# Performance work log

Measured on AMD Instinct MI355X. Metric: run time of the kernel, lower is better.

The kernel has to match this reference:

```python
import jax, jax.numpy as jnp
import numpy as np

DEPTH, HEADS, DIM_HEAD, DIM = 6, 16, 64, 1024
INNER = HEADS * DIM_HEAD  # 1024 == DIM
MLP = DIM                 # mlp_dim chosen == dim (see shape_source)
SCALE = DIM_HEAD ** -0.5
EPS = 1e-5


def _layernorm(x, w, b):
    m = jnp.mean(x, axis=-1, keepdims=True)
    v = jnp.mean(jnp.square(x - m), axis=-1, keepdims=True)
    return (x - m) * jax.lax.rsqrt(v + EPS) * w + b


def _rpq_weight(cb, codes):
    # cb: [G, 256, sub], codes: [out, G] -> W: [out, G*sub] == [out, in]
    G = cb.shape[0]
    W = cb[jnp.arange(G)[None, :], codes]  # [out, G, sub]
    return W.reshape(codes.shape[0], -1)


def _rpq_linear(x, cb, codes, b=None):
    W = _rpq_weight(cb, codes)
    y = jnp.einsum('bni,oi->bno', x, W)
    return y if b is None else y + b


def setup_inputs() -> dict:
    key = jax.random.key(0)
    ks = jax.random.split(key, 17)
    cs = 0.02  # codebook scale (kaiming-uniform-ish magnitude)
    return {
        'x': jax.random.normal(ks[0], (8, 1024, DIM), jnp.float32),
        'cb0': jax.random.normal(ks[1], (HEADS, 256, DIM // HEADS), jnp.float32) * cs,
        'cb1': jax.random.normal(ks[2], (HEADS, 256, DIM // HEADS), jnp.float32) * cs,
        'cb2': jax.random.normal(ks[3], (HEADS, 256, MLP // HEADS), jnp.float32) * cs,
        'cb3': jax.random.normal(ks[4], (HEADS, 256, MLP // HEADS), jnp.float32) * cs,
        'codes_qkv': jax.random.randint(ks[5], (DEPTH, 3 * INNER, HEADS), 0, 256, jnp.int32),
        'codes_out': jax.random.randint(ks[6], (DEPTH, DIM, HEADS), 0, 256, jnp.int32),
        'codes_fc1': jax.random.randint(ks[7], (DEPTH, MLP, HEADS), 0, 256, jnp.int32),
        'codes_fc2': jax.random.randint(ks[8], (DEPTH, DIM, HEADS), 0, 256, jnp.int32),
        'b_out': jax.random.normal(ks[9], (DEPTH, DIM), jnp.float32) * 0.02,
        'b_fc1': jax.random.normal(ks[10], (DEPTH, MLP), jnp.float32) * 0.02,
        'b_fc2': jax.random.normal(ks[11], (DEPTH, DIM), jnp.float32) * 0.02,
        'ln1_w': jax.random.uniform(ks[12], (DEPTH, DIM), jnp.float32, 0.5, 1.5),
        'ln1_b': jax.random.normal(ks[13], (DEPTH, DIM), jnp.float32) * 0.02,
        'ln2_w': jax.random.uniform(ks[14], (DEPTH, DIM), jnp.float32, 0.5, 1.5),
        'ln2_b': jax.random.normal(ks[15], (DEPTH, DIM), jnp.float32) * 0.02,
    }


def reference(x, cb0, cb1, cb2, cb3, codes_qkv, codes_out, codes_fc1, codes_fc2,
              b_out, b_fc1, b_fc2, ln1_w, ln1_b, ln2_w, ln2_b):
    b, n, _ = x.shape
    for i in range(DEPTH):
        # PreNorm Attention
        xn = _layernorm(x, ln1_w[i], ln1_b[i])
        qkv = _rpq_linear(xn, cb0, codes_qkv[i])  # [b, n, 3*INNER]
        q, k, v = jnp.split(qkv, 3, axis=-1)
        q = q.reshape(b, n, HEADS, DIM_HEAD).transpose(0, 2, 1, 3)  # bhnd
        k = k.reshape(b, n, HEADS, DIM_HEAD).transpose(0, 2, 1, 3)
        v = v.reshape(b, n, HEADS, DIM_HEAD).transpose(0, 2, 1, 3)
        dots = jnp.einsum('bhqd,bhkd->bhqk', q, k) * SCALE
        attn = jax.nn.softmax(dots, axis=-1)
        out = jnp.einsum('bhqk,bhkd->bhqd', attn, v)
        out = out.transpose(0, 2, 1, 3).reshape(b, n, INNER)
        out = _rpq_linear(out, cb1, codes_out[i], b_out[i])
        x = out + x
        # PreNorm FeedForward
        xn = _layernorm(x, ln2_w[i], ln2_b[i])
        h = jax.nn.gelu(_rpq_linear(xn, cb2, codes_fc1[i], b_fc1[i]), approximate=False)
        x = _rpq_linear(h, cb3, codes_fc2[i], b_fc2[i]) + x
    return x
```

## Files before the change

kernel.cpp:

```cpp
#include <hip/hip_runtime.h>
#include <hip/hip_bf16.h>


typedef __bf16 bf16x8 __attribute__((ext_vector_type(8)));
typedef __bf16 bf16x4 __attribute__((ext_vector_type(4)));
typedef float  f32x4  __attribute__((ext_vector_type(4)));
typedef float  f32x16 __attribute__((ext_vector_type(16)));
typedef unsigned int u32x4 __attribute__((ext_vector_type(4)));
typedef unsigned int u32_as1 __attribute__((address_space(1)));
typedef unsigned int u32_as3 __attribute__((address_space(3)));

#define MFMA16(a, b, c) __builtin_amdgcn_mfma_f32_16x16x32_bf16(a, b, c, 0, 0, 0)
#define MFMA32(a, b, c) __builtin_amdgcn_mfma_f32_32x32x16_bf16(a, b, c, 0, 0, 0)

__device__ __forceinline__ void gload16(void* lds, const void* g) {
  __builtin_amdgcn_global_load_lds((u32_as1*)(void*)g, (u32_as3*)lds, 16, 0, 0);
}

__device__ __forceinline__ unsigned pack2(float a, float b) {
  unsigned lo = (unsigned)__builtin_bit_cast(unsigned short, (__bf16)a);
  unsigned hi = (unsigned)__builtin_bit_cast(unsigned short, (__bf16)b);
  return lo | (hi << 16);
}
__device__ __forceinline__ void pswap(unsigned& a, unsigned& b) {
  asm("v_permlane32_swap_b32 %0, %1" : "+v"(a), "+v"(b));
}

__global__ __launch_bounds__(256) void dequant_kernel(
    __bf16* __restrict__ W,
    const float* __restrict__ cb0, const float* __restrict__ cb1,
    const float* __restrict__ cb2, const float* __restrict__ cb3,
    const int* __restrict__ codes_qkv, const int* __restrict__ codes_out,
    const int* __restrict__ codes_fc1, const int* __restrict__ codes_fc2)
{
  const int r = blockIdx.x;
  const int t = threadIdx.x;
  const float* cb; const int* cr;
  if (r < 3072)      { cb = cb0; cr = codes_qkv + r * 16; }
  else if (r < 4096) { cb = cb1; cr = codes_out + (r - 3072) * 16; }
  else if (r < 5120) { cb = cb2; cr = codes_fc1 + (r - 4096) * 16; }
  else               { cb = cb3; cr = codes_fc2 + (r - 5120) * 16; }
  const int g = t >> 4, j = (t & 15) * 4;
  const int code = cr[g];
  const float4 v = *(const float4*)(cb + ((size_t)(g * 256 + code) * 64) + j);
  bf16x4 o = { (__bf16)v.x, (__bf16)v.y, (__bf16)v.z, (__bf16)v.w };
  *(bf16x4*)(W + (size_t)r * 1024 + g * 64 + j) = o;
}

__global__ __launch_bounds__(256) void ln_kernel(
    const float* __restrict__ x, const float* __restrict__ w,
    const float* __restrict__ b, __bf16* __restrict__ out)
{
  const int row = blockIdx.x, t = threadIdx.x;
  const float4 v = *(const float4*)(x + (size_t)row * 1024 + t * 4);
  float s  = v.x + v.y + v.z + v.w;
  float sq = v.x * v.x + v.y * v.y + v.z * v.z + v.w * v.w;
  #pragma unroll
  for (int off = 32; off > 0; off >>= 1) {
    s  += __shfl_xor(s,  off, 64);
    sq += __shfl_xor(sq, off, 64);
  }
  __shared__ float red[8];
  const int wid = t >> 6, lane = t & 63;
  if (lane == 0) { red[wid] = s; red[4 + wid] = sq; }
  __syncthreads();
  s  = red[0] + red[1] + red[2] + red[3];
  sq = red[4] + red[5] + red[6] + red[7];
  const float mean = s * (1.0f / 1024.0f);
  const float var  = sq * (1.0f / 1024.0f) - mean * mean;
  const float rstd = rsqrtf(var + 1e-5f);
  const float4 wv = *(const float4*)(w + t * 4);
  const float4 bv = *(const float4*)(b + t * 4);
  bf16x4 o = { (__bf16)((v.x - mean) * rstd * wv.x + bv.x),
               (__bf16)((v.y - mean) * rstd * wv.y + bv.y),
               (__bf16)((v.z - mean) * rstd * wv.z + bv.z),
               (__bf16)((v.w - mean) * rstd * wv.w + bv.w) };
  *(bf16x4*)(out + (size_t)row * 1024 + t * 4) = o;
}

template<int EPI>
__global__ __launch_bounds__(256) void gemm_kernel(
    const __bf16* __restrict__ A, const __bf16* __restrict__ Bw,
    __bf16* __restrict__ oQ, __bf16* __restrict__ oK, __bf16* __restrict__ oVT,
    __bf16* __restrict__ oH, float* __restrict__ oX, const float* __restrict__ bias)
{
  __shared__ char smem[16384] __attribute__((aligned(128)));
  const int tid  = threadIdx.x;
  const int lane = tid & 63, wid = tid >> 6;
  const int l15 = lane & 15, l4 = lane >> 4;
  const int wr = wid >> 1, wc = wid & 1;
  const int m0 = blockIdx.x * 128, n0 = blockIdx.y * 128;

  const int srow = tid >> 2;
  const int scol = (tid & 3) * 8;

  f32x4 acc[4][4];
  #pragma unroll
  for (int i = 0; i < 4; ++i)
    #pragma unroll
    for (int j = 0; j < 4; ++j) acc[i][j] = (f32x4){0.f, 0.f, 0.f, 0.f};

  const __bf16* gA = A  + (size_t)(m0 + srow) * 1024 + scol;
  const __bf16* gB = Bw + (size_t)(n0 + srow) * 1024 + scol;
  char* ldsA0 = smem + wid * 1024;
  char* ldsA1 = smem + 4096  + wid * 1024;
  char* ldsB0 = smem + 8192  + wid * 1024;
  char* ldsB1 = smem + 12288 + wid * 1024;
  const int aoff = l15 * 64 + l4 * 16;

  for (int kk = 0; kk < 32; ++kk) {
    const int kb = kk * 32;
    gload16(ldsA0, gA + kb);
    gload16(ldsA1, gA + 64 * 1024 + kb);
    gload16(ldsB0, gB + kb);
    gload16(ldsB1, gB + 64 * 1024 + kb);
    __syncthreads();
    bf16x8 af[4], bfr[4];
    #pragma unroll
    for (int mi = 0; mi < 4; ++mi)
      af[mi] = *(const bf16x8*)(smem + (wr * 64 + mi * 16) * 64 + aoff);
    #pragma unroll
    for (int ni = 0; ni < 4; ++ni)
      bfr[ni] = *(const bf16x8*)(smem + 8192 + (wc * 64 + ni * 16) * 64 + aoff);
    #pragma unroll
    for (int mi = 0; mi < 4; ++mi)
      #pragma unroll
      for (int ni = 0; ni < 4; ++ni)
        acc[mi][ni] = MFMA16(af[mi], bfr[ni], acc[mi][ni]);
    __syncthreads();
  }

  #pragma unroll
  for (int mi = 0; mi < 4; ++mi) {
    #pragma unroll
    for (int ni = 0; ni < 4; ++ni) {
      const int n = n0 + wc * 64 + ni * 16 + l15;
      if constexpr (EPI == 0) {
        const int region = n >> 10, nn = n & 1023;
        const int hh = nn >> 6, d = nn & 63;
        const int m_base = m0 + wr * 64 + mi * 16 + l4 * 4;
        const int bb = m_base >> 10, s = m_base & 1023;
        if (region == 2) {
          bf16x4 pv = { (__bf16)acc[mi][ni][0], (__bf16)acc[mi][ni][1],
                        (__bf16)acc[mi][ni][2], (__bf16)acc[mi][ni][3] };
          *(bf16x4*)(oVT + ((size_t)(bb * 16 + hh) * 64 + d) * 1024 + s) = pv;
        } else {
          #pragma unroll
          for (int r = 0; r < 4; ++r) {
            const __bf16 bv = (__bf16)acc[mi][ni][r];
            if (region == 0) oQ[((size_t)(bb * 16 + hh) * 1024 + s + r) * 64 + d] = bv;
            else             oK[((size_t)(bb * 16 + hh) * 1024 + s + r) * 64 + d] = bv;
          }
        }
      } else {
        #pragma unroll
        for (int r = 0; r < 4; ++r) {
          const int m = m0 + wr * 64 + mi * 16 + l4 * 4 + r;
          const float v = acc[mi][ni][r];
          if constexpr (EPI == 1) {
            float* p = oX + (size_t)m * 1024 + n;
            *p = *p + v + bias[n];
          } else {
            float t = v + bias[n];
            t = 0.5f * t * (1.0f + erff(t * 0.70710678118f));
            oH[(size_t)m * 1024 + n] = (__bf16)t;
          }
        }
      }
    }
  }
}

__global__ __launch_bounds__(256) void attn_kernel(
    const __bf16* __restrict__ Q, const __bf16* __restrict__ K,
    const __bf16* __restrict__ VT, __bf16* __restrict__ AO)
{
  const int bh = blockIdx.x & 127;
  const int qt = blockIdx.x >> 7;
  const int tid = threadIdx.x, lane = tid & 63, wid = tid >> 6;
  const int l31 = lane & 31, hi = lane >> 5;
  const int q0 = qt * 128 + wid * 32;

  const __bf16* Qb = Q  + (size_t)bh * 65536;
  const __bf16* Kb = K  + (size_t)bh * 65536;
  const __bf16* Vb = VT + (size_t)bh * 65536;

  __shared__ char lds[2][16384] __attribute__((aligned(128)));

  const float ascale = 0.125f * 1.44269504089f;

  const int srow_in_chunk = lane >> 3;
  const int scol = (((lane & 7) ^ srow_in_chunk) << 3);

  #define STAGE(buf, kb_)                                                            \
    {                                                                                \
      _Pragma("unroll")                                                              \
      for (int ii = 0; ii < 4; ++ii) {                                               \
        const int i = wid + ii * 4;                                                  \
        const int chunk = i & 7;                                                     \
        const int row = chunk * 8 + srow_in_chunk;                                   \
        if (ii < 2) gload16((buf) + chunk * 1024,                                    \
                            Kb + (size_t)((kb_) + row) * 64 + scol);                 \
        else        gload16((buf) + 8192 + chunk * 1024,                             \
                            Vb + (size_t)row * 1024 + (kb_) + scol);                 \
      }                                                                              \
    }

  bf16x8 qf[4];
  #pragma unroll
  for (int c = 0; c < 4; ++c)
    qf[c] = *(const bf16x8*)(Qb + (size_t)(q0 + l31) * 64 + c * 16 + hi * 8);

  const u32x4 onesu = { 0x3f803f80u, 0x3f803f80u, 0x3f803f80u, 0x3f803f80u };
  const bf16x8 ones = __builtin_bit_cast(bf16x8, onesu);

  f32x16 o0, o1, sacc;
  #pragma unroll
  for (int r = 0; r < 16; ++r) { o0[r] = 0.f; o1[r] = 0.f; sacc[r] = 0.f; }
  float m = -1e30f;

  const int swz = (l31 & 7) << 4;

  STAGE(lds[0], 0);

  for (int kt = 0; kt < 16; ++kt) {
    __syncthreads();
    const char* Kl = lds[kt & 1];
    const char* Vl = lds[kt & 1] + 8192;
    if (kt < 15) STAGE(lds[(kt + 1) & 1], (kt + 1) * 64);

    f32x16 s0, s1;
    #pragma unroll
    for (int r = 0; r < 16; ++r) { s0[r] = 0.f; s1[r] = 0.f; }
    __builtin_amdgcn_s_setprio(1);
    #pragma unroll
    for (int c = 0; c < 4; ++c) {
      bf16x8 kf0 = *(const bf16x8*)(Kl + l31 * 128        + ((c * 32 + hi * 16) ^ swz));
      bf16x8 kf1 = *(const bf16x8*)(Kl + (32 + l31) * 128 + ((c * 32 + hi * 16) ^ swz));
      s0 = MFMA32(kf0, qf[c], s0);
      s1 = MFMA32(kf1, qf[c], s1);
    }
    __builtin_amdgcn_s_setprio(0);
    float t0 = fmaxf(s0[0], s0[1]),  t1 = fmaxf(s0[2], s0[3]);
    float t2 = fmaxf(s0[4], s0[5]),  t3 = fmaxf(s0[6], s0[7]);
    float t4 = fmaxf(s0[8], s0[9]),  t5 = fmaxf(s0[10], s0[11]);
    float t6 = fmaxf(s0[12], s0[13]), t7 = fmaxf(s0[14], s0[15]);
    float u0 = fmaxf(s1[0], s1[1]),  u1 = fmaxf(s1[2], s1[3]);
    float u2 = fmaxf(s1[4], s1[5]),  u3 = fmaxf(s1[6], s1[7]);
    float u4 = fmaxf(s1[8], s1[9]),  u5 = fmaxf(s1[10], s1[11]);
    float u6 = fmaxf(s1[12], s1[13]), u7 = fmaxf(s1[14], s1[15]);
    t0 = fmaxf(fmaxf(t0, t1), fmaxf(t2, t3));
    t4 = fmaxf(fmaxf(t4, t5), fmaxf(t6, t7));
    u0 = fmaxf(fmaxf(u0, u1), fmaxf(u2, u3));
    u4 = fmaxf(fmaxf(u4, u5), fmaxf(u6, u7));
    float pm = fmaxf(fmaxf(t0, t4), fmaxf(u0, u4));
    pm = fmaxf(pm, __shfl_xor(pm, 32, 64));
    const float pmx = pm * ascale;
    if (__any((int)(pmx > m + 8.0f))) {
      const float mnew = fmaxf(m, pmx);
      const float a = exp2f(m - mnew);
      m = mnew;
      #pragma unroll
      for (int r = 0; r < 16; ++r) {
        const float ab = __shfl(a, (r & 3) + 8 * (r >> 2) + 4 * hi, 64);
        o0[r] *= ab; o1[r] *= ab; sacc[r] *= ab;
      }
    }
    const float nm = -m;
    #pragma unroll
    for (int r = 0; r < 16; ++r) {
      s0[r] = exp2f(fmaf(s0[r], ascale, nm));
      s1[r] = exp2f(fmaf(s1[r], ascale, nm));
    }
    unsigned a0 = pack2(s0[0], s0[1]),   b0 = pack2(s0[4], s0[5]);
    unsigned a1 = pack2(s0[2], s0[3]),   b1 = pack2(s0[6], s0[7]);
    unsigned a2 = pack2(s0[8], s0[9]),   b2 = pack2(s0[12], s0[13]);
    unsigned a3 = pack2(s0[10], s0[11]), b3 = pack2(s0[14], s0[15]);
    unsigned c0 = pack2(s1[0], s1[1]),   d0 = pack2(s1[4], s1[5]);
    unsigned c1 = pack2(s1[2], s1[3]),   d1 = pack2(s1[6], s1[7]);
    unsigned c2 = pack2(s1[8], s1[9]),   d2 = pack2(s1[12], s1[13]);
    unsigned c3 = pack2(s1[10], s1[11]), d3 = pack2(s1[14], s1[15]);
    pswap(a0, b0); pswap(a1, b1); pswap(a2, b2); pswap(a3, b3);
    pswap(c0, d0); pswap(c1, d1); pswap(c2, d2); pswap(c3, d3);
    bf16x8 pfrag[4];
    pfrag[0] = __builtin_bit_cast(bf16x8, (u32x4){a0, a1, b0, b1});
    pfrag[1] = __builtin_bit_cast(bf16x8, (u32x4){a2, a3, b2, b3});
    pfrag[2] = __builtin_bit_cast(bf16x8, (u32x4){c0, c1, d0, d1});
    pfrag[3] = __builtin_bit_cast(bf16x8, (u32x4){c2, c3, d2, d3});
    __builtin_amdgcn_s_setprio(1);
    #pragma unroll
    for (int c = 0; c < 4; ++c) {
      bf16x8 v0 = *(const bf16x8*)(Vl + l31 * 128        + ((c * 32 + hi * 16) ^ swz));
      bf16x8 v1 = *(const bf16x8*)(Vl + (32 + l31) * 128 + ((c * 32 + hi * 16) ^ swz));
      o0 = MFMA32(pfrag[c], v0, o0);
      o1 = MFMA32(pfrag[c], v1, o1);
      sacc = MFMA32(pfrag[c], ones, sacc);
    }
    __builtin_amdgcn_s_setprio(0);
  }
  #undef STAGE

  const int bb = bh >> 4, hh = bh & 15;
  #pragma unroll
  for (int r = 0; r < 16; ++r) {
    const int crow = (r & 3) + 8 * (r >> 2) + 4 * hi;
    const float lb = 1.0f / sacc[r];
    const int srow = q0 + crow;
    AO[(size_t)(bb * 1024 + srow) * 1024 + hh * 64 + l31]      = (__bf16)(o0[r] * lb);
    AO[(size_t)(bb * 1024 + srow) * 1024 + hh * 64 + 32 + l31] = (__bf16)(o1[r] * lb);
  }
}

extern "C" void kernel_launch(void* const* d_in, const int* in_sizes, int n_in,
                              void* d_out, int out_size, void* d_ws, size_t ws_size,
                              hipStream_t stream)
{
  const float* x        = (const float*)d_in[0];
  const float* cb0      = (const float*)d_in[1];
  const float* cb1      = (const float*)d_in[2];
  const float* cb2      = (const float*)d_in[3];
  const float* cb3      = (const float*)d_in[4];
  const int* codes_qkv  = (const int*)d_in[5];
  const int* codes_out  = (const int*)d_in[6];
  const int* codes_fc1  = (const int*)d_in[7];
  const int* codes_fc2  = (const int*)d_in[8];
  const float* b_out    = (const float*)d_in[9];
  const float* b_fc1    = (const float*)d_in[10];
  const float* b_fc2    = (const float*)d_in[11];
  const float* ln1_w    = (const float*)d_in[12];
  const float* ln1_b    = (const float*)d_in[13];
  const float* ln2_w    = (const float*)d_in[14];
  const float* ln2_b    = (const float*)d_in[15];

  float* X = (float*)d_out;
  __bf16* ws = (__bf16*)d_ws;
  __bf16* W  = ws;
  __bf16* xn = ws + 6291456;
  __bf16* Qb = ws + 14680064;
  __bf16* Kb = ws + 23068672;
  __bf16* VT = ws + 31457280;
  __bf16* AO = ws + 39845888;
  __bf16* Hb = ws + 48234496;

  hipMemcpyAsync(X, x, (size_t)8192 * 1024 * 4, hipMemcpyDeviceToDevice, stream);

  for (int i = 0; i < 6; ++i) {
    dequant_kernel<<<6144, 256, 0, stream>>>(
        W, cb0, cb1, cb2, cb3,
        codes_qkv + (size_t)i * 3072 * 16, codes_out + (size_t)i * 1024 * 16,
        codes_fc1 + (size_t)i * 1024 * 16, codes_fc2 + (size_t)i * 1024 * 16);

    ln_kernel<<<8192, 256, 0, stream>>>(X, ln1_w + i * 1024, ln1_b + i * 1024, xn);

    gemm_kernel<0><<<dim3(64, 24), 256, 0, stream>>>(
        xn, W, Qb, Kb, VT, nullptr, nullptr, nullptr);

    attn_kernel<<<1024, 256, 0, stream>>>(Qb, Kb, VT, AO);

    gemm_kernel<1><<<dim3(64, 8), 256, 0, stream>>>(
        AO, W + (size_t)3072 * 1024, nullptr, nullptr, nullptr, nullptr, X, b_out + i * 1024);

    ln_kernel<<<8192, 256, 0, stream>>>(X, ln2_w + i * 1024, ln2_b + i * 1024, xn);

    gemm_kernel<2><<<dim3(64, 8), 256, 0, stream>>>(
        xn, W + (size_t)4096 * 1024, nullptr, nullptr, nullptr, Hb, nullptr, b_fc1 + i * 1024);

    gemm_kernel<1><<<dim3(64, 8), 256, 0, stream>>>(
        Hb, W + (size_t)5120 * 1024, nullptr, nullptr, nullptr, nullptr, X, b_fc2 + i * 1024);
  }
}
```

Before: 1.519 ms.

## Deepen GEMM K-tile, add XCD-aware block swizzle, widen attention blocks

The GEMM now stages a 64-wide K slice per iteration (32 KB LDS) and runs two MFMA sub-steps per sync, which halves the number of barriers. It also launches a 1D grid remapped with an XCD swizzle so that neighbouring tiles share L2. The attention kernel moves to 512-thread blocks covering 256 queries, so each K/V tile staged in LDS is reused by twice as many waves, with an adjusted swizzle to avoid bank conflicts. The costs are higher LDS use per block and possible occupancy changes.

```diff
diff --git a/kernel.cpp b/kernel.cpp
--- a/kernel.cpp
+++ b/kernel.cpp
@@ -24,6 +24,12 @@
 }
 __device__ __forceinline__ void pswap(unsigned& a, unsigned& b) {
   asm("v_permlane32_swap_b32 %0, %1" : "+v"(a), "+v"(b));
+}
+
+__device__ __forceinline__ int xcd_swizzle(int orig, int nwg) {
+  const int xcd = orig & 7, idx = orig >> 3;
+  const int q = nwg >> 3, r = nwg & 7;
+  return (xcd < r ? xcd * (q + 1) : r * (q + 1) + (xcd - r) * q) + idx;
 }
 
 __global__ __launch_bounds__(256) void dequant_kernel(
@@ -82,17 +88,19 @@
 __global__ __launch_bounds__(256) void gemm_kernel(
     const __bf16* __restrict__ A, const __bf16* __restrict__ Bw,
     __bf16* __restrict__ oQ, __bf16* __restrict__ oK, __bf16* __restrict__ oVT,
-    __bf16* __restrict__ oH, float* __restrict__ oX, const float* __restrict__ bias)
-{
-  __shared__ char smem[16384] __attribute__((aligned(128)));
+    __bf16* __restrict__ oH, float* __restrict__ oX, const float* __restrict__ bias,
+    int nTiles)
+{
+  __shared__ char smem[32768] __attribute__((aligned(128)));
   const int tid  = threadIdx.x;
   const int lane = tid & 63, wid = tid >> 6;
   const int l15 = lane & 15, l4 = lane >> 4;
   const int wr = wid >> 1, wc = wid & 1;
-  const int m0 = blockIdx.x * 128, n0 = blockIdx.y * 128;
-
-  const int srow = tid >> 2;
-  const int scol = (tid & 3) * 8;
+  const int wgid = xcd_swizzle(blockIdx.x, gridDim.x);
+  const int m0 = (wgid / nTiles) * 128, n0 = (wgid % nTiles) * 128;
+
+  const int srow8 = lane >> 3;
+  const int scole = (lane & 7) * 8;
 
   f32x4 acc[4][4];
   #pragma unroll
@@ -100,33 +108,33 @@
     #pragma unroll
     for (int j = 0; j < 4; ++j) acc[i][j] = (f32x4){0.f, 0.f, 0.f, 0.f};
 
-  const __bf16* gA = A  + (size_t)(m0 + srow) * 1024 + scol;
-  const __bf16* gB = Bw + (size_t)(n0 + srow) * 1024 + scol;
-  char* ldsA0 = smem + wid * 1024;
-  char* ldsA1 = smem + 4096  + wid * 1024;
-  char* ldsB0 = smem + 8192  + wid * 1024;
-  char* ldsB1 = smem + 12288 + wid * 1024;
-  const int aoff = l15 * 64 + l4 * 16;
-
-  for (int kk = 0; kk < 32; ++kk) {
-    const int kb = kk * 32;
-    gload16(ldsA0, gA + kb);
-    gload16(ldsA1, gA + 64 * 1024 + kb);
-    gload16(ldsB0, gB + kb);
-    gload16(ldsB1, gB + 64 * 1024 + kb);
+  const __bf16* gA = A  + (size_t)(m0 + srow8) * 1024 + scole;
+  const __bf16* gB = Bw + (size_t)(n0 + srow8) * 1024 + scole;
+
+  for (int kk = 0; kk < 16; ++kk) {
+    const int kb = kk * 64;
+    #pragma unroll
+    for (int ii = 0; ii < 4; ++ii) {
+      const int chunk = wid * 4 + ii;
+      gload16(smem + chunk * 1024,         gA + (size_t)chunk * 8192 + kb);
+      gload16(smem + 16384 + chunk * 1024, gB + (size_t)chunk * 8192 + kb);
+    }
     __syncthreads();
-    bf16x8 af[4], bfr[4];
-    #pragma unroll
-    for (int mi = 0; mi < 4; ++mi)
-      af[mi] = *(const bf16x8*)(smem + (wr * 64 + mi * 16) * 64 + aoff);
-    #pragma unroll
-    for (int ni = 0; ni < 4; ++ni)
-      bfr[ni] = *(const bf16x8*)(smem + 8192 + (wc * 64 + ni * 16) * 64 + aoff);
-    #pragma unroll
-    for (int mi = 0; mi < 4; ++mi)
+    #pragma unroll
+    for (int ks = 0; ks < 2; ++ks) {
+      bf16x8 af[4], bfr[4];
+      #pragma unroll
+      for (int mi = 0; mi < 4; ++mi)
+        af[mi] = *(const bf16x8*)(smem + (wr * 64 + mi * 16 + l15) * 128 + ks * 64 + l4 * 16);
       #pragma unroll
       for (int ni = 0; ni < 4; ++ni)
-        acc[mi][ni] = MFMA16(af[mi], bfr[ni], acc[mi][ni]);
+        bfr[ni] = *(const bf16x8*)(smem + 16384 + (wc * 64 + ni * 16 + l15) * 128 + ks * 64 + l4 * 16);
+      #pragma unroll
+      for (int mi = 0; mi < 4; ++mi)
+        #pragma unroll
+        for (int ni = 0; ni < 4; ++ni)
+          acc[mi][ni] = MFMA16(af[mi], bfr[ni], acc[mi][ni]);
+    }
     __syncthreads();
   }
 
@@ -171,7 +179,7 @@
   }
 }
 
-__global__ __launch_bounds__(256) void attn_kernel(
+__global__ __launch_bounds__(512, 4) void attn_kernel(
     const __bf16* __restrict__ Q, const __bf16* __restrict__ K,
     const __bf16* __restrict__ VT, __bf16* __restrict__ AO)
 {
@@ -179,7 +187,7 @@
   const int qt = blockIdx.x >> 7;
   const int tid = threadIdx.x, lane = tid & 63, wid = tid >> 6;
   const int l31 = lane & 31, hi = lane >> 5;
-  const int q0 = qt * 128 + wid * 32;
+  const int q0 = qt * 256 + wid * 32;
 
   const __bf16* Qb = Q  + (size_t)bh * 65536;
   const __bf16* Kb = K  + (size_t)bh * 65536;
@@ -190,20 +198,13 @@
   const float ascale = 0.125f * 1.44269504089f;
 
   const int srow_in_chunk = lane >> 3;
-  const int scol = (((lane & 7) ^ srow_in_chunk) << 3);
-
-  #define STAGE(buf, kb_)                                                            \
-    {                                                                                \
-      _Pragma("unroll")                                                              \
-      for (int ii = 0; ii < 4; ++ii) {                                               \
-        const int i = wid + ii * 4;                                                  \
-        const int chunk = i & 7;                                                     \
-        const int row = chunk * 8 + srow_in_chunk;                                   \
-        if (ii < 2) gload16((buf) + chunk * 1024,                                    \
-                            Kb + (size_t)((kb_) + row) * 64 + scol);                 \
-        else        gload16((buf) + 8192 + chunk * 1024,                             \
-                            Vb + (size_t)row * 1024 + (kb_) + scol);                 \
-      }                                                                              \
+  const int scol = (((lane & 7) ^ srow_in_chunk ^ (wid & 3)) << 3);
+
+  #define STAGE(buf, kb_)                                                       \
+    {                                                                           \
+      const int row_ = wid * 8 + srow_in_chunk;                                 \
+      gload16((buf) + wid * 1024, Kb + (size_t)((kb_) + row_) * 64 + scol);     \
+      gload16((buf) + 8192 + wid * 1024, Vb + (size_t)row_ * 1024 + (kb_) + scol); \
     }
 
   bf16x8 qf[4];
@@ -219,7 +220,7 @@
   for (int r = 0; r < 16; ++r) { o0[r] = 0.f; o1[r] = 0.f; sacc[r] = 0.f; }
   float m = -1e30f;
 
-  const int swz = (l31 & 7) << 4;
+  const int swz = (((l31 & 7) ^ ((l31 >> 3) & 3)) << 4);
 
   STAGE(lds[0], 0);
 
@@ -352,20 +353,20 @@
 
     ln_kernel<<<8192, 256, 0, stream>>>(X, ln1_w + i * 1024, ln1_b + i * 1024, xn);
 
-    gemm_kernel<0><<<dim3(64, 24), 256, 0, stream>>>(
-        xn, W, Qb, Kb, VT, nullptr, nullptr, nullptr);
-
-    attn_kernel<<<1024, 256, 0, stream>>>(Qb, Kb, VT, AO);
-
-    gemm_kernel<1><<<dim3(64, 8), 256, 0, stream>>>(
-        AO, W + (size_t)3072 * 1024, nullptr, nullptr, nullptr, nullptr, X, b_out + i * 1024);
+    gemm_kernel<0><<<1536, 256, 0, stream>>>(
+        xn, W, Qb, Kb, VT, nullptr, nullptr, nullptr, 24);
+
+    attn_kernel<<<512, 512, 0, stream>>>(Qb, Kb, VT, AO);
+
+    gemm_kernel<1><<<512, 256, 0, stream>>>(
+        AO, W + (size_t)3072 * 1024, nullptr, nullptr, nullptr, nullptr, X, b_out + i * 1024, 8);
 
     ln_kernel<<<8192, 256, 0, stream>>>(X, ln2_w + i * 1024, ln2_b + i * 1024, xn);
 
-    gemm_kernel<2><<<dim3(64, 8), 256, 0, stream>>>(
-        xn, W + (size_t)4096 * 1024, nullptr, nullptr, nullptr, Hb, nullptr, b_fc1 + i * 1024);
-
-    gemm_kernel<1><<<dim3(64, 8), 256, 0, stream>>>(
-        Hb, W + (size_t)5120 * 1024, nullptr, nullptr, nullptr, nullptr, X, b_fc2 + i * 1024);
-  }
-}
+    gemm_kernel<2><<<512, 256, 0, stream>>>(
+        xn, W + (size_t)4096 * 1024, nullptr, nullptr, nullptr, Hb, nullptr, b_fc1 + i * 1024, 8);
+
+    gemm_kernel<1><<<512, 256, 0, stream>>>(
+        Hb, W + (size_t)5120 * 1024, nullptr, nullptr, nullptr, nullptr, X, b_fc2 + i * 1024, 8);
+  }
+}
```

New measurement: 1.592 ms. +4.8%, slower.

## Use 8-wave attention blocks covering 256 queries with shared K/V staging

Applied to the files above, without the earlier changes.

Attention blocks grow from 4 to 8 waves, each block covering 256 query rows, so every K/V tile staged into LDS is reused by twice as many queries and total K/V global traffic halves. Each wave now issues one K and one V load per stage, and the LDS swizzle gains an extra XOR term by wave index to keep bank conflicts low. The row-max reduction is rewritten as three-input max chains so the compiler can emit max3 instructions. The trade-off is fewer blocks in flight (512 instead of 1024) and a 512-thread block that has to sync more waves at each barrier.

```diff
diff --git a/kernel.cpp b/kernel.cpp
--- a/kernel.cpp
+++ b/kernel.cpp
@@ -24,6 +24,9 @@
 }
 __device__ __forceinline__ void pswap(unsigned& a, unsigned& b) {
   asm("v_permlane32_swap_b32 %0, %1" : "+v"(a), "+v"(b));
+}
+__device__ __forceinline__ float max3f(float a, float b, float c) {
+  return fmaxf(fmaxf(a, b), c);
 }
 
 __global__ __launch_bounds__(256) void dequant_kernel(
@@ -171,7 +174,7 @@
   }
 }
 
-__global__ __launch_bounds__(256) void attn_kernel(
+__global__ __launch_bounds__(512, 4) void attn_kernel(
     const __bf16* __restrict__ Q, const __bf16* __restrict__ K,
     const __bf16* __restrict__ VT, __bf16* __restrict__ AO)
 {
@@ -179,7 +182,7 @@
   const int qt = blockIdx.x >> 7;
   const int tid = threadIdx.x, lane = tid & 63, wid = tid >> 6;
   const int l31 = lane & 31, hi = lane >> 5;
-  const int q0 = qt * 128 + wid * 32;
+  const int q0 = qt * 256 + wid * 32;
 
   const __bf16* Qb = Q  + (size_t)bh * 65536;
   const __bf16* Kb = K  + (size_t)bh * 65536;
@@ -190,20 +193,13 @@
   const float ascale = 0.125f * 1.44269504089f;
 
   const int srow_in_chunk = lane >> 3;
-  const int scol = (((lane & 7) ^ srow_in_chunk) << 3);
-
-  #define STAGE(buf, kb_)                                                            \
-    {                                                                                \
-      _Pragma("unroll")                                                              \
-      for (int ii = 0; ii < 4; ++ii) {                                               \
-        const int i = wid + ii * 4;                                                  \
-        const int chunk = i & 7;                                                     \
-        const int row = chunk * 8 + srow_in_chunk;                                   \
-        if (ii < 2) gload16((buf) + chunk * 1024,                                    \
-                            Kb + (size_t)((kb_) + row) * 64 + scol);                 \
-        else        gload16((buf) + 8192 + chunk * 1024,                             \
-                            Vb + (size_t)row * 1024 + (kb_) + scol);                 \
-      }                                                                              \
+  const int scol = (((lane & 7) ^ srow_in_chunk ^ (wid & 3)) << 3);
+
+  #define STAGE(buf, kb_)                                                       \
+    {                                                                           \
+      const int row_ = wid * 8 + srow_in_chunk;                                 \
+      gload16((buf) + wid * 1024, Kb + (size_t)((kb_) + row_) * 64 + scol);     \
+      gload16((buf) + 8192 + wid * 1024, Vb + (size_t)row_ * 1024 + (kb_) + scol); \
     }
 
   bf16x8 qf[4];
@@ -219,7 +215,7 @@
   for (int r = 0; r < 16; ++r) { o0[r] = 0.f; o1[r] = 0.f; sacc[r] = 0.f; }
   float m = -1e30f;
 
-  const int swz = (l31 & 7) << 4;
+  const int swz = (((l31 & 7) ^ ((l31 >> 3) & 3)) << 4);
 
   STAGE(lds[0], 0);
 
@@ -241,19 +237,21 @@
       s1 = MFMA32(kf1, qf[c], s1);
     }
     __builtin_amdgcn_s_setprio(0);
-    float t0 = fmaxf(s0[0], s0[1]),  t1 = fmaxf(s0[2], s0[3]);
-    float t2 = fmaxf(s0[4], s0[5]),  t3 = fmaxf(s0[6], s0[7]);
-    float t4 = fmaxf(s0[8], s0[9]),  t5 = fmaxf(s0[10], s0[11]);
-    float t6 = fmaxf(s0[12], s0[13]), t7 = fmaxf(s0[14], s0[15]);
-    float u0 = fmaxf(s1[0], s1[1]),  u1 = fmaxf(s1[2], s1[3]);
-    float u2 = fmaxf(s1[4], s1[5]),  u3 = fmaxf(s1[6], s1[7]);
-    float u4 = fmaxf(s1[8], s1[9]),  u5 = fmaxf(s1[10], s1[11]);
-    float u6 = fmaxf(s1[12], s1[13]), u7 = fmaxf(s1[14], s1[15]);
-    t0 = fmaxf(fmaxf(t0, t1), fmaxf(t2, t3));
-    t4 = fmaxf(fmaxf(t4, t5), fmaxf(t6, t7));
-    u0 = fmaxf(fmaxf(u0, u1), fmaxf(u2, u3));
-    u4 = fmaxf(fmaxf(u4, u5), fmaxf(u6, u7));
-    float pm = fmaxf(fmaxf(t0, t4), fmaxf(u0, u4));
+    float p0 = max3f(s0[0],  s0[1],  s0[2]);
+    float p1 = max3f(s0[3],  s0[4],  s0[5]);
+    float p2 = max3f(s0[6],  s0[7],  s0[8]);
+    float p3 = max3f(s0[9],  s0[10], s0[11]);
+    float p4 = max3f(s0[12], s0[13], s0[14]);
+    float q1_ = max3f(s1[0],  s1[1],  s1[2]);
+    float q2_ = max3f(s1[3],  s1[4],  s1[5]);
+    float q3_ = max3f(s1[6],  s1[7],  s1[8]);
+    float q4_ = max3f(s1[9],  s1[10], s1[11]);
+    float q5_ = max3f(s1[12], s1[13], s1[14]);
+    float ta = max3f(p0, p1, p2);
+    float tb = max3f(p3, p4, s0[15]);
+    float tc = max3f(q1_, q2_, q3_);
+    float td = max3f(q4_, q5_, s1[15]);
+    float pm = fmaxf(fmaxf(ta, tb), fmaxf(tc, td));
     pm = fmaxf(pm, __shfl_xor(pm, 32, 64));
     const float pmx = pm * ascale;
     if (__any((int)(pmx > m + 8.0f))) {
@@ -355,7 +353,7 @@
     gemm_kernel<0><<<dim3(64, 24), 256, 0, stream>>>(
         xn, W, Qb, Kb, VT, nullptr, nullptr, nullptr);
 
-    attn_kernel<<<1024, 256, 0, stream>>>(Qb, Kb, VT, AO);
+    attn_kernel<<<512, 512, 0, stream>>>(Qb, Kb, VT, AO);
 
     gemm_kernel<1><<<dim3(64, 8), 256, 0, stream>>>(
         AO, W + (size_t)3072 * 1024, nullptr, nullptr, nullptr, nullptr, X, b_out + i * 1024);
```

Measured after the change: 1.499 ms. No clear change (-1.3%).
